# Kernel optimization log

Hardware: AMD Instinct MI355X
Metric: run time of the kernel (lower is better)

## Reference

```python
import jax, jax.numpy as jnp
import numpy as np

B, T, D, H = 64, 1024, 512, 512
_SCALE = 1.0 / np.sqrt(H)  # torch-style RNNCell init scale


def setup_inputs() -> dict:
    key = jax.random.key(0)
    ks = jax.random.split(key, 9)
    f32 = jnp.float32
    return {
        "x": jax.random.normal(ks[0], (B, T, D), dtype=f32),
        "Wih_f": jax.random.normal(ks[1], (H, D), dtype=f32) * _SCALE,
        "Whh_f": jax.random.normal(ks[2], (H, H), dtype=f32) * _SCALE,
        "bih_f": jax.random.normal(ks[3], (H,), dtype=f32) * _SCALE,
        "bhh_f": jax.random.normal(ks[4], (H,), dtype=f32) * _SCALE,
        "Wih_b": jax.random.normal(ks[5], (H, D), dtype=f32) * _SCALE,
        "Whh_b": jax.random.normal(ks[6], (H, H), dtype=f32) * _SCALE,
        "bih_b": jax.random.normal(ks[7], (H,), dtype=f32) * _SCALE,
        "bhh_b": jax.random.normal(ks[8], (H,), dtype=f32) * _SCALE,
    }


def _scan_direction(x_bt, Wih, Whh, bih, bhh):
    # x_bt: [B, T, D] already in processing order for this direction.
    # Precompute the input projection for all timesteps (one big GEMM),
    # leaving only the recurrent GEMM inside the scan.
    xp = jnp.einsum('btd,hd->bth', x_bt, Wih) + bih + bhh  # [B, T, H]
    h0 = jnp.zeros((x_bt.shape[0], Whh.shape[0]), dtype=x_bt.dtype)

    def step(h, xt):  # xt: [B, H]
        h_new = jnp.tanh(xt + h @ Whh.T)
        return h_new, h_new

    _, hs = jax.lax.scan(step, h0, jnp.swapaxes(xp, 0, 1))  # hs: [T, B, H]
    return jnp.swapaxes(hs, 0, 1)  # [B, T, H] in processing order


def reference(x, Wih_f, Whh_f, bih_f, bhh_f, Wih_b, Whh_b, bih_b, bhh_b):
    # Forward direction: timesteps 0..T-1.
    fh = _scan_direction(x, Wih_f, Whh_f, bih_f, bhh_f)
    # Backward direction: cell consumes x reversed in time; torch code appends
    # hiddens in processing order (i.e., index t <-> original time T-1-t).
    bh = _scan_direction(x[:, ::-1, :], Wih_b, Whh_b, bih_b, bhh_b)
    # output_last=False branch: [B, 2, T, H]
    return jnp.stack([fh, bh], axis=1)
```

## Files before the change

### kernel.cpp

```cpp
#include <hip/hip_runtime.h>
#include <hip/hip_fp16.h>
#include <cstdint>

typedef _Float16 h2 __attribute__((ext_vector_type(2)));
typedef _Float16 h8 __attribute__((ext_vector_type(8)));
typedef float    f4 __attribute__((ext_vector_type(4)));
typedef uint32_t u4 __attribute__((ext_vector_type(4)));

#define BATCH 64
#define TSTEPS 1024
#define DDIM 512
#define HDIM 512

static __device__ __forceinline__ float fdot2(uint32_t w, uint32_t h, float acc) {
  return __builtin_amdgcn_fdot2(__builtin_bit_cast(h2, w), __builtin_bit_cast(h2, h), acc, false);
}

__global__ void prep_kernel(const float* __restrict__ Wih_f, const float* __restrict__ Whh_f,
                            const float* __restrict__ bih_f, const float* __restrict__ bhh_f,
                            const float* __restrict__ Wih_b, const float* __restrict__ Whh_b,
                            const float* __restrict__ bih_b, const float* __restrict__ bhh_b,
                            _Float16* __restrict__ wi16, uint32_t* __restrict__ whT,
                            float* __restrict__ bsum) {
  int i = blockIdx.x * 256 + threadIdx.x;
  if (i < 2 * 512 * 512) {
    const float* s = (i < 512 * 512) ? Wih_f : Wih_b;
    wi16[i] = (_Float16)s[i & (512 * 512 - 1)];
  }
  if (i < 2 * 256 * 512) {
    int d = i >> 17; int rem = i & ((1 << 17) - 1);
    int kp = rem >> 9; int j = rem & 511;
    const float* W = d ? Whh_b : Whh_f;
    h2 p; p[0] = (_Float16)W[j * 512 + 2 * kp]; p[1] = (_Float16)W[j * 512 + 2 * kp + 1];
    whT[i] = __builtin_bit_cast(uint32_t, p);
  }
  if (i < 2 * 512) {
    int d = i >> 9, j = i & 511;
    bsum[i] = d ? (bih_b[j] + bhh_b[j]) : (bih_f[j] + bhh_f[j]);
  }
}

__global__ __launch_bounds__(256) void xp_gemm(const float* __restrict__ x,
                                               const _Float16* __restrict__ wi,
                                               const float* __restrict__ bsum,
                                               _Float16* __restrict__ xp) {
  __shared__ _Float16 As[128][40];
  __shared__ _Float16 Bs[128][40];
  const int mt = blockIdx.x, nt = blockIdx.y, dir = blockIdx.z;
  const int m0 = mt * 128, n0 = nt * 128;
  const int tid = threadIdx.x;
  const int lane = tid & 63, w = tid >> 6;
  const int wr = w >> 1, wc = w & 1;
  const int ra = tid >> 1, hf = tid & 1;

  const int mrow = m0 + ra;
  const int bb = mrow >> 10, pp = mrow & 1023;
  const int srow = dir ? ((bb << 10) + (1023 - pp)) : mrow;
  const float*    xbase = x + (size_t)srow * 512 + hf * 16;
  const _Float16* wbase = wi + (size_t)dir * 512 * 512 + (size_t)(n0 + ra) * 512 + hf * 16;

  f4 acc[4][4];
  #pragma unroll
  for (int a = 0; a < 4; ++a)
    #pragma unroll
    for (int b = 0; b < 4; ++b) acc[a][b] = (f4)0.f;

  for (int k0 = 0; k0 < 512; k0 += 32) {
    f4 x0 = *(const f4*)(xbase + k0);
    f4 x1 = *(const f4*)(xbase + k0 + 4);
    f4 x2 = *(const f4*)(xbase + k0 + 8);
    f4 x3 = *(const f4*)(xbase + k0 + 12);
    h8 b0 = *(const h8*)(wbase + k0);
    h8 b1 = *(const h8*)(wbase + k0 + 8);
    h8 a0, a1;
    #pragma unroll
    for (int u = 0; u < 4; ++u) {
      a0[u] = (_Float16)x0[u]; a0[4 + u] = (_Float16)x1[u];
      a1[u] = (_Float16)x2[u]; a1[4 + u] = (_Float16)x3[u];
    }
    __syncthreads();
    *(h8*)&As[ra][hf * 16]     = a0;
    *(h8*)&As[ra][hf * 16 + 8] = a1;
    *(h8*)&Bs[ra][hf * 16]     = b0;
    *(h8*)&Bs[ra][hf * 16 + 8] = b1;
    __syncthreads();
    h8 af[4], bf[4];
    #pragma unroll
    for (int fm = 0; fm < 4; ++fm)
      af[fm] = *(const h8*)&As[wr * 64 + fm * 16 + (lane & 15)][(lane >> 4) * 8];
    #pragma unroll
    for (int fn = 0; fn < 4; ++fn)
      bf[fn] = *(const h8*)&Bs[wc * 64 + fn * 16 + (lane & 15)][(lane >> 4) * 8];
    #pragma unroll
    for (int fm = 0; fm < 4; ++fm)
      #pragma unroll
      for (int fn = 0; fn < 4; ++fn)
        acc[fm][fn] = __builtin_amdgcn_mfma_f32_16x16x32_f16(af[fm], bf[fn], acc[fm][fn], 0, 0, 0);
  }

  float bsv[4];
  #pragma unroll
  for (int fn = 0; fn < 4; ++fn)
    bsv[fn] = bsum[dir * 512 + n0 + wc * 64 + fn * 16 + (lane & 15)];
  #pragma unroll
  for (int fm = 0; fm < 4; ++fm)
    #pragma unroll
    for (int fn = 0; fn < 4; ++fn)
      #pragma unroll
      for (int u = 0; u < 4; ++u) {
        int m = m0 + wr * 64 + fm * 16 + (lane >> 4) * 4 + u;
        int n = n0 + wc * 64 + fn * 16 + (lane & 15);
        xp[((size_t)dir << 25) + (size_t)m * 512 + n] = (_Float16)(acc[fm][fn][u] + bsv[fn]);
      }
}

__global__ __launch_bounds__(1024) void rnn_rec(const _Float16* __restrict__ xp,
                                                const uint32_t* __restrict__ whT,
                                                float* __restrict__ out) {
  extern __shared__ char smem[];
  uint32_t* wl   = (uint32_t*)smem;
  uint32_t* hl   = (uint32_t*)(smem + 131072);
  float*    psum = (float*)(smem + 132096);

  const int bid = blockIdx.x;
  const int dir = bid & 1, b = bid >> 1;
  const int l = threadIdx.x;
  const int q = l >> 8, r = l & 255;
  const uint32_t* wbase = whT + dir * (256 * 512);

  uint32_t w0[64], w1[32];
  #pragma unroll
  for (int p = 0; p < 64; ++p) w0[p] = wbase[(q * 64 + p) * 512 + r];
  #pragma unroll
  for (int p = 0; p < 32; ++p) w1[p] = wbase[(q * 64 + p) * 512 + 256 + r];
  #pragma unroll
  for (int p = 32; p < 64; ++p) wl[(p - 32) * 1024 + l] = wbase[(q * 64 + p) * 512 + 256 + r];
  if (l < 256) hl[l] = 0;
  __syncthreads();

  const _Float16* xpb = xp + ((size_t)(dir * 64 + b) << 19);
  float* op = out + ((size_t)(b * 2 + dir) << 19);

  for (int t = 0; t < TSTEPS; ++t) {
    float xpv = 0.f;
    if (l < 512) xpv = (float)xpb[t * 512 + l];
    float acc0 = 0.f, acc1 = 0.f;
    #pragma unroll
    for (int c = 0; c < 16; ++c) {
      u4 hq = *(const u4*)(hl + q * 64 + c * 4);
      if (c < 8) {
        #pragma unroll
        for (int i2 = 0; i2 < 4; ++i2) {
          acc0 = fdot2(w0[c * 4 + i2], hq[i2], acc0);
          acc1 = fdot2(w1[c * 4 + i2], hq[i2], acc1);
        }
      } else {
        #pragma unroll
        for (int i2 = 0; i2 < 4; ++i2) {
          uint32_t wv = wl[((c - 8) * 4 + i2) * 1024 + l];
          acc0 = fdot2(w0[c * 4 + i2], hq[i2], acc0);
          acc1 = fdot2(wv, hq[i2], acc1);
        }
      }
    }
    psum[q * 520 + r]       = acc0;
    psum[q * 520 + 256 + r] = acc1;
    __syncthreads();
    if (l < 512) {
      float s = psum[l] + psum[520 + l] + psum[1040 + l] + psum[1560 + l] + xpv;
      float e = __expf(2.f * s);
      float hv = 1.f - 2.f * __builtin_amdgcn_rcpf(e + 1.f);
      op[t * 512 + l] = hv;
      ((_Float16*)hl)[l] = (_Float16)hv;
    }
    __syncthreads();
  }
}

extern "C" void kernel_launch(void* const* d_in, const int* in_sizes, int n_in,
                              void* d_out, int out_size, void* d_ws, size_t ws_size,
                              hipStream_t stream) {
  const float* x     = (const float*)d_in[0];
  const float* Wih_f = (const float*)d_in[1];
  const float* Whh_f = (const float*)d_in[2];
  const float* bih_f = (const float*)d_in[3];
  const float* bhh_f = (const float*)d_in[4];
  const float* Wih_b = (const float*)d_in[5];
  const float* Whh_b = (const float*)d_in[6];
  const float* bih_b = (const float*)d_in[7];
  const float* bhh_b = (const float*)d_in[8];

  char* ws = (char*)d_ws;
  _Float16* xp16 = (_Float16*)ws;
  _Float16* wi16 = (_Float16*)(ws + 134217728);
  uint32_t* whT  = (uint32_t*)(ws + 135266304);
  float*    bsum = (float*)(ws + 136314880);
  float* out = (float*)d_out;

  prep_kernel<<<2048, 256, 0, stream>>>(Wih_f, Whh_f, bih_f, bhh_f,
                                        Wih_b, Whh_b, bih_b, bhh_b, wi16, whT, bsum);
  dim3 g(512, 4, 2);
  xp_gemm<<<g, 256, 0, stream>>>(x, wi16, bsum, xp16);

  const int REC_LDS = 140416;
  hipFuncSetAttribute((const void*)rnn_rec, hipFuncAttributeMaxDynamicSharedMemorySize, REC_LDS);
  rnn_rec<<<128, 1024, REC_LDS, stream>>>(xp16, whT, out);
}
```

Baseline: 1.938 ms.

## Keep full recurrent weight in registers with 8-way K split per block

After: 2.959 ms. 1.53x slower.

```diff
diff --git a/kernel.cpp b/kernel.cpp
--- a/kernel.cpp
+++ b/kernel.cpp
@@ -114,63 +114,65 @@
       }
 }
 
-__global__ __launch_bounds__(1024) void rnn_rec(const _Float16* __restrict__ xp,
-                                                const uint32_t* __restrict__ whT,
-                                                float* __restrict__ out) {
-  extern __shared__ char smem[];
-  uint32_t* wl   = (uint32_t*)smem;
-  uint32_t* hl   = (uint32_t*)(smem + 131072);
-  float*    psum = (float*)(smem + 132096);
+__global__ __launch_bounds__(1024, 4) void rnn_rec(const _Float16* __restrict__ xp,
+                                                   const uint32_t* __restrict__ whT,
+                                                   float* __restrict__ out) {
+  __shared__ uint32_t hl[256];
+  __shared__ float psum[8][512];
 
   const int bid = blockIdx.x;
   const int dir = bid & 1, b = bid >> 1;
   const int l = threadIdx.x;
-  const int q = l >> 8, r = l & 255;
-  const uint32_t* wbase = whT + dir * (256 * 512);
-
-  uint32_t w0[64], w1[32];
-  #pragma unroll
-  for (int p = 0; p < 64; ++p) w0[p] = wbase[(q * 64 + p) * 512 + r];
-  #pragma unroll
-  for (int p = 0; p < 32; ++p) w1[p] = wbase[(q * 64 + p) * 512 + 256 + r];
-  #pragma unroll
-  for (int p = 32; p < 64; ++p) wl[(p - 32) * 1024 + l] = wbase[(q * 64 + p) * 512 + 256 + r];
+  const int ks = l >> 7, r = l & 127;
+
+  const uint32_t* wb = whT + dir * (256 * 512) + (ks * 32) * 512 + r;
+  uint32_t w0[32], w1[32], w2[32], w3[32];
+  #pragma unroll
+  for (int p = 0; p < 32; ++p) w0[p] = wb[p * 512];
+  #pragma unroll
+  for (int p = 0; p < 32; ++p) w1[p] = wb[p * 512 + 128];
+  #pragma unroll
+  for (int p = 0; p < 32; ++p) w2[p] = wb[p * 512 + 256];
+  #pragma unroll
+  for (int p = 0; p < 32; ++p) w3[p] = wb[p * 512 + 384];
+
   if (l < 256) hl[l] = 0;
   __syncthreads();
 
-  const _Float16* xpb = xp + ((size_t)(dir * 64 + b) << 19);
-  float* op = out + ((size_t)(b * 2 + dir) << 19);
+  const _Float16* xpp = xp + ((size_t)dir << 25) + ((size_t)b << 19);
+  float* op = out + (((size_t)(b * 2 + dir)) << 19);
 
   for (int t = 0; t < TSTEPS; ++t) {
     float xpv = 0.f;
-    if (l < 512) xpv = (float)xpb[t * 512 + l];
-    float acc0 = 0.f, acc1 = 0.f;
-    #pragma unroll
-    for (int c = 0; c < 16; ++c) {
-      u4 hq = *(const u4*)(hl + q * 64 + c * 4);
-      if (c < 8) {
-        #pragma unroll
-        for (int i2 = 0; i2 < 4; ++i2) {
-          acc0 = fdot2(w0[c * 4 + i2], hq[i2], acc0);
-          acc1 = fdot2(w1[c * 4 + i2], hq[i2], acc1);
-        }
-      } else {
-        #pragma unroll
-        for (int i2 = 0; i2 < 4; ++i2) {
-          uint32_t wv = wl[((c - 8) * 4 + i2) * 1024 + l];
-          acc0 = fdot2(w0[c * 4 + i2], hq[i2], acc0);
-          acc1 = fdot2(wv, hq[i2], acc1);
-        }
+    if (l < 512) xpv = (float)xpp[(size_t)t * 512 + l];
+
+    float a0 = 0.f, a1 = 0.f, a2 = 0.f, a3 = 0.f;
+    const uint32_t* hq = hl + ks * 32;
+    #pragma unroll
+    for (int cb = 0; cb < 8; ++cb) {
+      u4 hv4 = *(const u4*)(hq + cb * 4);
+      #pragma unroll
+      for (int i = 0; i < 4; ++i) {
+        uint32_t hw = hv4[i];
+        a0 = fdot2(w0[cb * 4 + i], hw, a0);
+        a1 = fdot2(w1[cb * 4 + i], hw, a1);
+        a2 = fdot2(w2[cb * 4 + i], hw, a2);
+        a3 = fdot2(w3[cb * 4 + i], hw, a3);
       }
     }
-    psum[q * 520 + r]       = acc0;
-    psum[q * 520 + 256 + r] = acc1;
-    __syncthreads();
+    psum[ks][r]       = a0;
+    psum[ks][r + 128] = a1;
+    psum[ks][r + 256] = a2;
+    psum[ks][r + 384] = a3;
+    __syncthreads();
+
     if (l < 512) {
-      float s = psum[l] + psum[520 + l] + psum[1040 + l] + psum[1560 + l] + xpv;
+      float s = xpv;
+      #pragma unroll
+      for (int k2 = 0; k2 < 8; ++k2) s += psum[k2][l];
       float e = __expf(2.f * s);
       float hv = 1.f - 2.f * __builtin_amdgcn_rcpf(e + 1.f);
-      op[t * 512 + l] = hv;
+      op[(size_t)t * 512 + l] = hv;
       ((_Float16*)hl)[l] = (_Float16)hv;
     }
     __syncthreads();
@@ -202,7 +204,5 @@
   dim3 g(512, 4, 2);
   xp_gemm<<<g, 256, 0, stream>>>(x, wi16, bsum, xp16);
 
-  const int REC_LDS = 140416;
-  hipFuncSetAttribute((const void*)rnn_rec, hipFuncAttributeMaxDynamicSharedMemorySize, REC_LDS);
-  rnn_rec<<<128, 1024, REC_LDS, stream>>>(xp16, whT, out);
-}
+  rnn_rec<<<128, 1024, 0, stream>>>(xp16, whT, out);
+}
```
